# Performance work log

Hardware: AMD Instinct MI355X
Metric: run time of the kernel (lower is better)

Reference implementation:

```python
import jax, jax.numpy as jnp
import numpy as np
import math

N_EMBD = 1024
N_HEAD = 16
N_CTX = 2048
SCALE = True
NEG = 1e10


def setup_inputs() -> dict:
    key = jax.random.key(0)
    ks = jax.random.split(key, 4)
    B, S = 2, 2048
    x = jax.random.normal(ks[0], (B, S, N_EMBD), dtype=jnp.float32)
    c_attn_w = jax.random.normal(ks[1], (N_EMBD, 3 * N_EMBD), dtype=jnp.float32) * 0.02
    c_attn_b = jnp.zeros((3 * N_EMBD,), dtype=jnp.float32)
    c_proj_w = jax.random.normal(ks[2], (N_EMBD, N_EMBD), dtype=jnp.float32) * 0.02
    c_proj_b = jnp.zeros((N_EMBD,), dtype=jnp.float32)
    return {"x": x, "c_attn_w": c_attn_w, "c_attn_b": c_attn_b,
            "c_proj_w": c_proj_w, "c_proj_b": c_proj_b}


def reference(x, c_attn_w, c_attn_b, c_proj_w, c_proj_b):
    B, S, D = x.shape
    H = N_HEAD
    hd = D // H
    qkv = x @ c_attn_w + c_attn_b                      # [B,S,3D]
    q, k, v = jnp.split(qkv, 3, axis=-1)
    # split heads -> [B,H,S,hd]
    q = q.reshape(B, S, H, hd).transpose(0, 2, 1, 3)
    k = k.reshape(B, S, H, hd).transpose(0, 2, 1, 3)
    v = v.reshape(B, S, H, hd).transpose(0, 2, 1, 3)
    w = jnp.einsum('bhqd,bhkd->bhqk', q, k)           # [B,H,S,S]
    if SCALE:
        w = w / math.sqrt(hd)
    # multiplicative causal mask trick: w*b - 1e10*(1-b)
    b = jnp.tril(jnp.ones((S, S), dtype=w.dtype))[None, None]
    w = w * b - NEG * (1.0 - b)
    w = jax.nn.softmax(w, axis=-1)
    a = jnp.einsum('bhqk,bhkd->bhqd', w, v)           # [B,H,S,hd]
    a = a.transpose(0, 2, 1, 3).reshape(B, S, D)      # merge heads
    a = a @ c_proj_w + c_proj_b
    present = jnp.stack((k, v))                       # [2,B,H,S,hd]
    return a, present
```

## Files before the change

kernel.cpp:

```cpp
#include <hip/hip_runtime.h>
#include <hip/hip_bf16.h>
#include <cstdint>
#include <cstddef>

#define SEQ 2048
#define DMODEL 1024
#define NHEAD 16
#define HDIM 64
#define MTOT 4096
#define NQKV 3072
#define KDIM 1024

#define OUT_K_BASE  4194304u
#define OUT_V_BASE  8388608u

#define QSCALE 0.18033688011112043f

typedef __attribute__((ext_vector_type(4))) float f32x4;
typedef __attribute__((ext_vector_type(8))) __bf16 bf16x8;
typedef __attribute__((ext_vector_type(8))) short s16x8;
typedef __attribute__((ext_vector_type(4))) short s16x4;
typedef __attribute__((ext_vector_type(4))) int i32x4;

static __device__ __forceinline__ unsigned short f2bf(float f) {
  unsigned int u = __builtin_bit_cast(unsigned int, f);
  u += 0x7FFFu + ((u >> 16) & 1u);
  return (unsigned short)(u >> 16);
}

static __device__ __forceinline__ s16x4 pack4(float4 v) {
  s16x4 r;
  r[0] = (short)f2bf(v.x);
  r[1] = (short)f2bf(v.y);
  r[2] = (short)f2bf(v.z);
  r[3] = (short)f2bf(v.w);
  return r;
}

static __device__ __forceinline__ int cvtpk(float lo, float hi) {
  int r;
  asm("v_cvt_pk_bf16_f32 %0, %1, %2" : "=v"(r) : "v"(lo), "v"(hi));
  return r;
}

static __device__ __forceinline__ f32x4 mfma16(s16x8 a, s16x8 b, f32x4 c) {
  return __builtin_amdgcn_mfma_f32_16x16x32_bf16(
      __builtin_bit_cast(bf16x8, a), __builtin_bit_cast(bf16x8, b), c, 0, 0, 0);
}

static __device__ __forceinline__ void gload16(const void* g, void* l) {
  __builtin_amdgcn_global_load_lds(
      (const __attribute__((address_space(1))) unsigned int*)(uintptr_t)g,
      (__attribute__((address_space(3))) unsigned int*)(uintptr_t)l,
      16, 0, 0);
}

__global__ __launch_bounds__(256) void convert_x(
    const float* __restrict__ X, unsigned short* __restrict__ Xbf)
{
  int i = blockIdx.x * 256 + threadIdx.x;
  float4 v = reinterpret_cast<const float4*>(X)[i];
  reinterpret_cast<s16x4*>(Xbf)[i] = pack4(v);
}

__global__ __launch_bounds__(256) void convert_wt(
    const float* __restrict__ W, unsigned short* __restrict__ Wt, int N)
{
  __shared__ unsigned short t[64][72];
  const int n0 = blockIdx.x * 64, k0 = blockIdx.y * 64;
  const int tid = threadIdx.x;
#pragma unroll
  for (int i = 0; i < 4; ++i) {
    int f = tid + (i << 8);
    int r = f >> 4, c4 = (f & 15) << 2;
    float4 v = *reinterpret_cast<const float4*>(&W[(size_t)(k0 + r) * N + n0 + c4]);
    *reinterpret_cast<s16x4*>(&t[r][c4]) = pack4(v);
  }
  __syncthreads();
#pragma unroll
  for (int i = 0; i < 2; ++i) {
    int g = tid + (i << 8);
    int n = g >> 3, k8 = (g & 7) << 3;
    s16x8 o;
#pragma unroll
    for (int jj = 0; jj < 8; ++jj) o[jj] = (short)t[k8 + jj][n];
    *reinterpret_cast<s16x8*>(&Wt[(size_t)(n0 + n) * KDIM + k0 + k8]) = o;
  }
}

#define GEMM_MAIN_LOOP(Aptr, Btptr)                                           \
  const int tid = threadIdx.x;                                                \
  const int lane = tid & 63;                                                  \
  const int wv = tid >> 6;                                                    \
  const int wr = wv >> 1, wc = wv & 1;                                        \
  const int m0 = blockIdx.x * 128;                                            \
  const int n0 = blockIdx.y * 128;                                            \
  const int lr = lane & 15;                                                   \
  const int gq = lane >> 4;                                                   \
  const f32x4 fzero = {0.f, 0.f, 0.f, 0.f};                                   \
  f32x4 acc[4][4];                                                            \
  _Pragma("unroll") for (int i = 0; i < 4; ++i)                               \
      _Pragma("unroll") for (int j = 0; j < 4; ++j) acc[i][j] = fzero;        \
  {                                                                           \
    const int ar0 = tid >> 2, ac0 = (tid & 3) << 3;                           \
    const int ar1 = (tid + 256) >> 2, ac1 = (tid & 3) << 3;                   \
    const int ub0 = wv << 9;                                                  \
    const int ub1 = 2048 + (wv << 9);                                         \
                                        \
    auto stage = [&](int nb, int kk) {                                        \
      gload16(&(Aptr)[(size_t)(m0 + ar0) * KDIM + kk + ac0],                  \
              &lds_a[nb][0][0] + ub0);                                        \
      gload16(&(Aptr)[(size_t)(m0 + ar1) * KDIM + kk + ac1],                  \
              &lds_a[nb][0][0] + ub1);                                        \
      gload16(&(Btptr)[(size_t)(n0 + ar0) * KDIM + kk + ac0],                 \
              &lds_b[nb][0][0] + ub0);                                        \
      gload16(&(Btptr)[(size_t)(n0 + ar1) * KDIM + kk + ac1],                 \
              &lds_b[nb][0][0] + ub1);                                        \
    };                                                                        \
    stage(0, 0);                                                              \
    for (int t = 0; t < 32; ++t) {                                            \
      __syncthreads();              \
      if (t < 31) stage((t + 1) & 1, (t + 1) << 5);                           \
      const int bufg = t & 1;                                                 \
      s16x8 af[4], bfv[4];                                                    \
      _Pragma("unroll") for (int mi = 0; mi < 4; ++mi)                        \
          af[mi] = *reinterpret_cast<const s16x8*>(                           \
              &lds_a[bufg][wr * 64 + mi * 16 + lr][gq << 3]);                 \
      _Pragma("unroll") for (int ni = 0; ni < 4; ++ni)                        \
          bfv[ni] = *reinterpret_cast<const s16x8*>(                          \
              &lds_b[bufg][wc * 64 + ni * 16 + lr][gq << 3]);                 \
      _Pragma("unroll") for (int ni = 0; ni < 4; ++ni)                        \
          _Pragma("unroll") for (int mi = 0; mi < 4; ++mi)                    \
              acc[mi][ni] = mfma16(af[mi], bfv[ni], acc[mi][ni]);             \
    }                                                                         \
  }

__global__ __launch_bounds__(256) void qkv_gemm(
    const unsigned short* __restrict__ Xbf,
    const unsigned short* __restrict__ Wt,
    const float* __restrict__ Bias,
    float* out,
    unsigned short* __restrict__ Qbf)
{
  __shared__ __align__(16) unsigned short lds_a[2][128][32];
  __shared__ __align__(16) unsigned short lds_b[2][128][32];

  unsigned short* Kbf = (unsigned short*)out;
  unsigned short* Vt  = Kbf + 4194304;

  GEMM_MAIN_LOOP(Xbf, Wt)

#pragma unroll
  for (int ni = 0; ni < 4; ++ni) {
    int c = n0 + wc * 64 + ni * 16 + lr;
    float bias = Bias[c];
    int seg = c >> 10;
    int cc = c & 1023;
    int h = cc >> 6, d = cc & 63;
#pragma unroll
    for (int mi = 0; mi < 4; ++mi) {
#pragma unroll
      for (int j = 0; j < 4; ++j) {
        int m = m0 + wr * 64 + mi * 16 + gq * 4 + j;
        int b = m >> 11, s = m & 2047;
        float val = acc[mi][ni][j] + bias;
        size_t idx = (size_t)((b * NHEAD + h) * SEQ + s) * HDIM + d;
        if (seg == 0) {
          Qbf[idx] = f2bf(val * QSCALE);
        } else if (seg == 1) {
          out[OUT_K_BASE + idx] = val;
          Kbf[idx] = f2bf(val);
        } else {
          out[OUT_V_BASE + idx] = val;
          Vt[((size_t)(b * NHEAD + h) * HDIM + d) * SEQ + s] = f2bf(val);
        }
      }
    }
  }
}

__global__ __launch_bounds__(256) void proj_gemm(
    const unsigned short* __restrict__ Abf,
    const unsigned short* __restrict__ Wpt,
    const float* __restrict__ Bias,
    float* __restrict__ out)
{
  __shared__ __align__(16) unsigned short lds_a[2][128][32];
  __shared__ __align__(16) unsigned short lds_b[2][128][32];

  GEMM_MAIN_LOOP(Abf, Wpt)

#pragma unroll
  for (int ni = 0; ni < 4; ++ni) {
    int c = n0 + wc * 64 + ni * 16 + lr;
    float bias = Bias[c];
#pragma unroll
    for (int mi = 0; mi < 4; ++mi) {
#pragma unroll
      for (int j = 0; j < 4; ++j) {
        int m = m0 + wr * 64 + mi * 16 + gq * 4 + j;
        out[(size_t)m * DMODEL + c] = acc[mi][ni][j] + bias;
      }
    }
  }
}

__global__ __launch_bounds__(256) void attn_fwd(
    const unsigned short* __restrict__ Qbf,
    const unsigned short* __restrict__ Kbf,
    const unsigned short* __restrict__ Vtg,
    unsigned short* __restrict__ Abf)
{
  __shared__ __align__(16) unsigned short K_lds[2][64][64];
  __shared__ __align__(16) unsigned short V_lds[2][64][64];

  const int tid = threadIdx.x;
  const int lane = tid & 63;
  const int wv = tid >> 6;
  const int bid = blockIdx.x;
  const int qt = 31 - (bid >> 5);
  const int bh = bid & 31;

  const int lr = lane & 15;
  const int gq = lane >> 4;

  const unsigned short* Kg = Kbf + (size_t)bh * (SEQ * HDIM);
  const unsigned short* Vg = Vtg + (size_t)bh * (SEQ * HDIM);
  const unsigned short* Qg = Qbf + (size_t)bh * (SEQ * HDIM)
                                 + (size_t)(qt * 64 + wv * 16) * HDIM;

  s16x8 qf0 = *reinterpret_cast<const s16x8*>(&Qg[lr * 64 + (gq << 3)]);
  s16x8 qf1 = *reinterpret_cast<const s16x8*>(&Qg[lr * 64 + 32 + (gq << 3)]);

  const f32x4 fzero = {0.f, 0.f, 0.f, 0.f};
  f32x4 O[4];
  float mrow = -1e30f, lrow = 0.f;
#pragma unroll
  for (int ni = 0; ni < 4; ++ni) O[ni] = fzero;

#define STAGE(kv0, nb)                                                        \
  {                                                                           \
    _Pragma("unroll")                                                         \
    for (int i = 0; i < 2; ++i) {                                             \
      int L = tid + (i << 8);                                                 \
      int r = L >> 3, c = L & 7;                                              \
      int cc = (c ^ (r & 7)) << 3;                                            \
      int ubase = ((i << 8) + (wv << 6)) << 3;                                \
      gload16(&Kg[(((kv0) + r) << 6) + cc], &K_lds[nb][0][0] + ubase);        \
      gload16(&Vg[((size_t)r << 11) + (kv0) + cc], &V_lds[nb][0][0] + ubase); \
    }                                                                         \
  }

  STAGE(0, 0);

  for (int t = 0; t <= qt; ++t) {
    __syncthreads();
    if (t < qt) STAGE((t + 1) * 64, (t + 1) & 1);
    const int buf = t & 1;

    f32x4 sc[4];
#pragma unroll
    for (int ni = 0; ni < 4; ++ni) {
      int kr = ni * 16 + lr;
      int sw = kr & 7;
      s16x8 kb0 = *reinterpret_cast<const s16x8*>(&K_lds[buf][kr][(gq ^ sw) << 3]);
      s16x8 kb1 = *reinterpret_cast<const s16x8*>(&K_lds[buf][kr][((gq + 4) ^ sw) << 3]);
      f32x4 tacc = mfma16(kb0, qf0, fzero);
      sc[ni] = mfma16(kb1, qf1, tacc);
    }

    if (t == qt) {
      int qloc = wv * 16 + lr;
#pragma unroll
      for (int ni = 0; ni < 4; ++ni)
#pragma unroll
        for (int r = 0; r < 4; ++r)
          if (ni * 16 + gq * 4 + r > qloc) sc[ni][r] = -1e30f;
    }

    float tmax = fmaxf(fmaxf(fmaxf(sc[0][0], sc[0][1]), fmaxf(sc[0][2], sc[0][3])),
                       fmaxf(fmaxf(sc[1][0], sc[1][1]), fmaxf(sc[1][2], sc[1][3])));
    tmax = fmaxf(tmax,
                 fmaxf(fmaxf(fmaxf(sc[2][0], sc[2][1]), fmaxf(sc[2][2], sc[2][3])),
                       fmaxf(fmaxf(sc[3][0], sc[3][1]), fmaxf(sc[3][2], sc[3][3]))));
    tmax = fmaxf(tmax, __shfl_xor(tmax, 16));
    tmax = fmaxf(tmax, __shfl_xor(tmax, 32));
    float newm = fmaxf(mrow, tmax);
    float fs = __builtin_amdgcn_exp2f(mrow - newm);
    mrow = newm;
    float rs = 0.f;
#pragma unroll
    for (int ni = 0; ni < 4; ++ni) {
#pragma unroll
      for (int r = 0; r < 4; ++r) {
        float p = __builtin_amdgcn_exp2f(sc[ni][r] - newm);
        sc[ni][r] = p;
        rs += p;
      }
    }
    rs += __shfl_xor(rs, 16);
    rs += __shfl_xor(rs, 32);
    lrow = lrow * fs + rs;
#pragma unroll
    for (int ni = 0; ni < 4; ++ni) O[ni] *= fs;

    int pk[4][2];
#pragma unroll
    for (int ni = 0; ni < 4; ++ni) {
      pk[ni][0] = cvtpk(sc[ni][0], sc[ni][1]);
      pk[ni][1] = cvtpk(sc[ni][2], sc[ni][3]);
    }
    const int srcA = lr + ((lane & 16) << 1);
    const int srcB = srcA + 16;
    const bool lowhalf = (gq < 2);
    s16x8 pB[2];
#pragma unroll
    for (int h = 0; h < 2; ++h) {
      int y0 = __shfl(pk[2 * h][0], srcA);
      int y1 = __shfl(pk[2 * h][1], srcA);
      int y2 = __shfl(pk[2 * h][0], srcB);
      int y3 = __shfl(pk[2 * h][1], srcB);
      int z0 = __shfl(pk[2 * h + 1][0], srcA);
      int z1 = __shfl(pk[2 * h + 1][1], srcA);
      int z2 = __shfl(pk[2 * h + 1][0], srcB);
      int z3 = __shfl(pk[2 * h + 1][1], srcB);
      i32x4 dw;
      dw[0] = lowhalf ? y0 : z0;
      dw[1] = lowhalf ? y1 : z1;
      dw[2] = lowhalf ? y2 : z2;
      dw[3] = lowhalf ? y3 : z3;
      pB[h] = __builtin_bit_cast(s16x8, dw);
    }

#pragma unroll
    for (int ni = 0; ni < 4; ++ni) {
      int dr = ni * 16 + lr;
      int sw = dr & 7;
      s16x8 vb0 = *reinterpret_cast<const s16x8*>(&V_lds[buf][dr][(gq ^ sw) << 3]);
      s16x8 vb1 = *reinterpret_cast<const s16x8*>(&V_lds[buf][dr][((gq + 4) ^ sw) << 3]);
      O[ni] = mfma16(vb0, pB[0], O[ni]);
      O[ni] = mfma16(vb1, pB[1], O[ni]);
    }
  }

  const int b = bh >> 4, h = bh & 15;
  float inv = 1.0f / lrow;
  int srow = qt * 64 + wv * 16 + lr;
  size_t base = (size_t)(b * SEQ + srow) * DMODEL + h * 64 + (gq << 2);
#pragma unroll
  for (int ni = 0; ni < 4; ++ni) {
    s16x4 ov;
#pragma unroll
    for (int r = 0; r < 4; ++r) ov[r] = (short)f2bf(O[ni][r] * inv);
    *reinterpret_cast<s16x4*>(&Abf[base + ni * 16]) = ov;
  }
#undef STAGE
}

extern "C" void kernel_launch(void* const* d_in, const int* in_sizes, int n_in,
                              void* d_out, int out_size, void* d_ws, size_t ws_size,
                              hipStream_t stream) {
  const float* x        = (const float*)d_in[0];
  const float* c_attn_w = (const float*)d_in[1];
  const float* c_attn_b = (const float*)d_in[2];
  const float* c_proj_w = (const float*)d_in[3];
  const float* c_proj_b = (const float*)d_in[4];
  float* out = (float*)d_out;

  unsigned short* Qbf = (unsigned short*)d_ws;
  unsigned short* Xbf = Qbf + 4194304;
  unsigned short* Abf = Xbf;
  unsigned short* Wt  = Qbf + 8388608;
  unsigned short* Wpt = Wt;
  unsigned short* Kbf = (unsigned short*)out;
  unsigned short* Vt  = Kbf + 4194304;

  convert_x<<<dim3(4096), 256, 0, stream>>>(x, Xbf);
  convert_wt<<<dim3(48, 16), 256, 0, stream>>>(c_attn_w, Wt, NQKV);
  qkv_gemm<<<dim3(32, 24), 256, 0, stream>>>(Xbf, Wt, c_attn_b, out, Qbf);
  convert_wt<<<dim3(16, 16), 256, 0, stream>>>(c_proj_w, Wpt, DMODEL);
  attn_fwd<<<dim3(1024), 256, 0, stream>>>(Qbf, Kbf, Vt, Abf);
  proj_gemm<<<dim3(32, 8), 256, 0, stream>>>(Abf, Wpt, c_proj_b, out);
}
```

Baseline: 132.9 us.

## Swizzle GEMM LDS tiles, LDS-transpose V epilogue, and stage P through LDS

Applies an XOR swizzle to the GEMM LDS A/B tiles to reduce bank conflicts on fragment reads. The QKV epilogue is split per segment, and the V segment is transposed through LDS so that Vt is written with coalesced 16-byte stores instead of strided scalar writes. In attention, the P matrix is re-laid out through a per-wave swizzled LDS buffer instead of a chain of cross-lane shuffles, and launch bounds request 4 blocks per CU. This adds LDS traffic and extra shared memory, which could limit occupancy.

```diff
diff --git a/kernel.cpp b/kernel.cpp
--- a/kernel.cpp
+++ b/kernel.cpp
@@ -20,7 +20,7 @@
 typedef __attribute__((ext_vector_type(8))) __bf16 bf16x8;
 typedef __attribute__((ext_vector_type(8))) short s16x8;
 typedef __attribute__((ext_vector_type(4))) short s16x4;
-typedef __attribute__((ext_vector_type(4))) int i32x4;
+typedef __attribute__((ext_vector_type(2))) int i32x2;
 
 static __device__ __forceinline__ unsigned short f2bf(float f) {
   unsigned int u = __builtin_bit_cast(unsigned int, f);
@@ -102,22 +102,23 @@
   _Pragma("unroll") for (int i = 0; i < 4; ++i)                               \
       _Pragma("unroll") for (int j = 0; j < 4; ++j) acc[i][j] = fzero;        \
   {                                                                           \
-    const int ar0 = tid >> 2, ac0 = (tid & 3) << 3;                           \
-    const int ar1 = (tid + 256) >> 2, ac1 = (tid & 3) << 3;                   \
+    const int ar0 = tid >> 2;                                                 \
+    const int ar1 = ar0 + 64;                                                 \
+    const int ac0 = (((tid & 3) ^ ((ar0 >> 1) & 3)) << 3);                    \
     const int ub0 = wv << 9;                                                  \
     const int ub1 = 2048 + (wv << 9);                                         \
-                                        \
     auto stage = [&](int nb, int kk) {                                        \
       gload16(&(Aptr)[(size_t)(m0 + ar0) * KDIM + kk + ac0],                  \
               &lds_a[nb][0][0] + ub0);                                        \
-      gload16(&(Aptr)[(size_t)(m0 + ar1) * KDIM + kk + ac1],                  \
+      gload16(&(Aptr)[(size_t)(m0 + ar1) * KDIM + kk + ac0],                  \
               &lds_a[nb][0][0] + ub1);                                        \
       gload16(&(Btptr)[(size_t)(n0 + ar0) * KDIM + kk + ac0],                 \
               &lds_b[nb][0][0] + ub0);                                        \
-      gload16(&(Btptr)[(size_t)(n0 + ar1) * KDIM + kk + ac1],                 \
+      gload16(&(Btptr)[(size_t)(n0 + ar1) * KDIM + kk + ac0],                 \
               &lds_b[nb][0][0] + ub1);                                        \
     };                                                                        \
     stage(0, 0);                                                              \
+    const int fsw = ((lr >> 1) & 3);                                          \
     for (int t = 0; t < 32; ++t) {                                            \
       __syncthreads();              \
       if (t < 31) stage((t + 1) & 1, (t + 1) << 5);                           \
@@ -125,10 +126,10 @@
       s16x8 af[4], bfv[4];                                                    \
       _Pragma("unroll") for (int mi = 0; mi < 4; ++mi)                        \
           af[mi] = *reinterpret_cast<const s16x8*>(                           \
-              &lds_a[bufg][wr * 64 + mi * 16 + lr][gq << 3]);                 \
+              &lds_a[bufg][wr * 64 + mi * 16 + lr][(gq ^ fsw) << 3]);         \
       _Pragma("unroll") for (int ni = 0; ni < 4; ++ni)                        \
           bfv[ni] = *reinterpret_cast<const s16x8*>(                          \
-              &lds_b[bufg][wc * 64 + ni * 16 + lr][gq << 3]);                 \
+              &lds_b[bufg][wc * 64 + ni * 16 + lr][(gq ^ fsw) << 3]);         \
       _Pragma("unroll") for (int ni = 0; ni < 4; ++ni)                        \
           _Pragma("unroll") for (int mi = 0; mi < 4; ++mi)                    \
               acc[mi][ni] = mfma16(af[mi], bfv[ni], acc[mi][ni]);             \
@@ -150,31 +151,74 @@
 
   GEMM_MAIN_LOOP(Xbf, Wt)
 
-#pragma unroll
-  for (int ni = 0; ni < 4; ++ni) {
-    int c = n0 + wc * 64 + ni * 16 + lr;
-    float bias = Bias[c];
-    int seg = c >> 10;
-    int cc = c & 1023;
-    int h = cc >> 6, d = cc & 63;
-#pragma unroll
-    for (int mi = 0; mi < 4; ++mi) {
-#pragma unroll
-      for (int j = 0; j < 4; ++j) {
-        int m = m0 + wr * 64 + mi * 16 + gq * 4 + j;
-        int b = m >> 11, s = m & 2047;
-        float val = acc[mi][ni][j] + bias;
-        size_t idx = (size_t)((b * NHEAD + h) * SEQ + s) * HDIM + d;
-        if (seg == 0) {
-          Qbf[idx] = f2bf(val * QSCALE);
-        } else if (seg == 1) {
+  const int seg = n0 >> 10;
+
+  if (seg == 0) {
+#pragma unroll
+    for (int ni = 0; ni < 4; ++ni) {
+      int c = n0 + wc * 64 + ni * 16 + lr;
+      float bias = Bias[c];
+      int h = (c & 1023) >> 6, d = c & 63;
+#pragma unroll
+      for (int mi = 0; mi < 4; ++mi)
+#pragma unroll
+        for (int j = 0; j < 4; ++j) {
+          int m = m0 + wr * 64 + mi * 16 + gq * 4 + j;
+          int b = m >> 11, s = m & 2047;
+          Qbf[(size_t)((b * NHEAD + h) * SEQ + s) * HDIM + d] =
+              f2bf((acc[mi][ni][j] + bias) * QSCALE);
+        }
+    }
+  } else if (seg == 1) {
+#pragma unroll
+    for (int ni = 0; ni < 4; ++ni) {
+      int c = n0 + wc * 64 + ni * 16 + lr;
+      float bias = Bias[c];
+      int h = (c & 1023) >> 6, d = c & 63;
+#pragma unroll
+      for (int mi = 0; mi < 4; ++mi)
+#pragma unroll
+        for (int j = 0; j < 4; ++j) {
+          int m = m0 + wr * 64 + mi * 16 + gq * 4 + j;
+          int b = m >> 11, s = m & 2047;
+          float val = acc[mi][ni][j] + bias;
+          size_t idx = (size_t)((b * NHEAD + h) * SEQ + s) * HDIM + d;
           out[OUT_K_BASE + idx] = val;
           Kbf[idx] = f2bf(val);
-        } else {
-          out[OUT_V_BASE + idx] = val;
-          Vt[((size_t)(b * NHEAD + h) * HDIM + d) * SEQ + s] = f2bf(val);
         }
-      }
+    }
+  } else {
+    __syncthreads();
+    unsigned short* T = (wv < 2) ? (&lds_a[0][0][0] + (wv << 12))
+                                 : (&lds_b[0][0][0] + ((wv - 2) << 12));
+    const int b = m0 >> 11;
+    const int s0 = (m0 & 2047) + wr * 64;
+    const int h = (n0 >> 6) - 32 + wc;
+#pragma unroll
+    for (int ni = 0; ni < 4; ++ni) {
+      int c = n0 + wc * 64 + ni * 16 + lr;
+      float bias = Bias[c];
+      int d_loc = ni * 16 + lr;
+      int dsw = d_loc & 7;
+#pragma unroll
+      for (int mi = 0; mi < 4; ++mi)
+#pragma unroll
+        for (int j = 0; j < 4; ++j) {
+          int s_loc = mi * 16 + gq * 4 + j;
+          float val = acc[mi][ni][j] + bias;
+          out[OUT_V_BASE +
+              (size_t)((b * NHEAD + h) * SEQ + s0 + s_loc) * HDIM + d_loc] = val;
+          T[d_loc * 64 + ((((s_loc >> 3) ^ dsw)) << 3) + (s_loc & 7)] = f2bf(val);
+        }
+    }
+#pragma unroll
+    for (int it = 0; it < 8; ++it) {
+      int dl = (lane >> 3) + (it << 3);
+      int cl = lane & 7;
+      s16x8 vv = *reinterpret_cast<const s16x8*>(
+          &T[dl * 64 + ((cl ^ (dl & 7)) << 3)]);
+      size_t vi = (((size_t)(b * NHEAD + h) * HDIM + dl) << 11) + s0 + (cl << 3);
+      *reinterpret_cast<s16x8*>(&Vt[vi]) = vv;
     }
   }
 }
@@ -205,7 +249,7 @@
   }
 }
 
-__global__ __launch_bounds__(256) void attn_fwd(
+__global__ __launch_bounds__(256, 4) void attn_fwd(
     const unsigned short* __restrict__ Qbf,
     const unsigned short* __restrict__ Kbf,
     const unsigned short* __restrict__ Vtg,
@@ -213,6 +257,7 @@
 {
   __shared__ __align__(16) unsigned short K_lds[2][64][64];
   __shared__ __align__(16) unsigned short V_lds[2][64][64];
+  __shared__ __align__(16) unsigned short P_lds[4][16][64];
 
   const int tid = threadIdx.x;
   const int lane = tid & 63;
@@ -236,7 +281,7 @@
   f32x4 O[4];
   float mrow = -1e30f, lrow = 0.f;
 #pragma unroll
-  for (int ni = 0; ni < 4; ++ni) O[ni] = fzero;
+  for (int no = 0; no < 4; ++no) O[no] = fzero;
 
 #define STAGE(kv0, nb)                                                        \
   {                                                                           \
@@ -302,44 +347,31 @@
     rs += __shfl_xor(rs, 32);
     lrow = lrow * fs + rs;
 #pragma unroll
-    for (int ni = 0; ni < 4; ++ni) O[ni] *= fs;
-
-    int pk[4][2];
-#pragma unroll
-    for (int ni = 0; ni < 4; ++ni) {
-      pk[ni][0] = cvtpk(sc[ni][0], sc[ni][1]);
-      pk[ni][1] = cvtpk(sc[ni][2], sc[ni][3]);
-    }
-    const int srcA = lr + ((lane & 16) << 1);
-    const int srcB = srcA + 16;
-    const bool lowhalf = (gq < 2);
-    s16x8 pB[2];
-#pragma unroll
-    for (int h = 0; h < 2; ++h) {
-      int y0 = __shfl(pk[2 * h][0], srcA);
-      int y1 = __shfl(pk[2 * h][1], srcA);
-      int y2 = __shfl(pk[2 * h][0], srcB);
-      int y3 = __shfl(pk[2 * h][1], srcB);
-      int z0 = __shfl(pk[2 * h + 1][0], srcA);
-      int z1 = __shfl(pk[2 * h + 1][1], srcA);
-      int z2 = __shfl(pk[2 * h + 1][0], srcB);
-      int z3 = __shfl(pk[2 * h + 1][1], srcB);
-      i32x4 dw;
-      dw[0] = lowhalf ? y0 : z0;
-      dw[1] = lowhalf ? y1 : z1;
-      dw[2] = lowhalf ? y2 : z2;
-      dw[3] = lowhalf ? y3 : z3;
-      pB[h] = __builtin_bit_cast(s16x8, dw);
-    }
-
-#pragma unroll
-    for (int ni = 0; ni < 4; ++ni) {
-      int dr = ni * 16 + lr;
-      int sw = dr & 7;
-      s16x8 vb0 = *reinterpret_cast<const s16x8*>(&V_lds[buf][dr][(gq ^ sw) << 3]);
-      s16x8 vb1 = *reinterpret_cast<const s16x8*>(&V_lds[buf][dr][((gq + 4) ^ sw) << 3]);
-      O[ni] = mfma16(vb0, pB[0], O[ni]);
-      O[ni] = mfma16(vb1, pB[1], O[ni]);
+    for (int no = 0; no < 4; ++no) O[no] *= fs;
+
+    {
+      unsigned short* Prow = &P_lds[wv][lr][0];
+      const int swl = lr & 7;
+#pragma unroll
+      for (int ni = 0; ni < 4; ++ni) {
+        i32x2 d2;
+        d2[0] = cvtpk(sc[ni][0], sc[ni][1]);
+        d2[1] = cvtpk(sc[ni][2], sc[ni][3]);
+        int off = ((((2 * ni) + (gq >> 1)) ^ swl) << 3) + ((gq & 1) << 2);
+        *reinterpret_cast<i32x2*>(&Prow[off]) = d2;
+      }
+      s16x8 pB0 = *reinterpret_cast<const s16x8*>(&Prow[(gq ^ swl) << 3]);
+      s16x8 pB1 = *reinterpret_cast<const s16x8*>(&Prow[((gq + 4) ^ swl) << 3]);
+
+#pragma unroll
+      for (int no = 0; no < 4; ++no) {
+        int dr = no * 16 + lr;
+        int sw = dr & 7;
+        s16x8 vb0 = *reinterpret_cast<const s16x8*>(&V_lds[buf][dr][(gq ^ sw) << 3]);
+        s16x8 vb1 = *reinterpret_cast<const s16x8*>(&V_lds[buf][dr][((gq + 4) ^ sw) << 3]);
+        O[no] = mfma16(vb0, pB0, O[no]);
+        O[no] = mfma16(vb1, pB1, O[no]);
+      }
     }
   }
 
@@ -348,11 +380,11 @@
   int srow = qt * 64 + wv * 16 + lr;
   size_t base = (size_t)(b * SEQ + srow) * DMODEL + h * 64 + (gq << 2);
 #pragma unroll
-  for (int ni = 0; ni < 4; ++ni) {
+  for (int no = 0; no < 4; ++no) {
     s16x4 ov;
 #pragma unroll
-    for (int r = 0; r < 4; ++r) ov[r] = (short)f2bf(O[ni][r] * inv);
-    *reinterpret_cast<s16x4*>(&Abf[base + ni * 16]) = ov;
+    for (int r = 0; r < 4; ++r) ov[r] = (short)f2bf(O[no][r] * inv);
+    *reinterpret_cast<s16x4*>(&Abf[base + no * 16]) = ov;
   }
 #undef STAGE
 }
```

Measured after the change: 120.3 us. 1.1x faster.
